# Performance work log

Measured on AMD Instinct MI355X. Metric: run time of the kernel, lower is better.

## Reference

```python
import jax, jax.numpy as jnp
from jax import lax
import numpy as np

B, T, I, H = 256, 1024, 128, 256


def setup_inputs() -> dict:
    key = jax.random.key(0)
    k1, k2, k3 = jax.random.split(key, 3)
    # Xavier-ish scaling so sigmoid/tanh gates are not saturated
    s_ih = float(np.sqrt(2.0 / (I + 3 * H)))
    s_hh = float(np.sqrt(2.0 / (H + 3 * H)))
    return {
        "x": jax.random.normal(k1, (B, T, I), dtype=jnp.float32),
        "h0": jnp.zeros((B, H), dtype=jnp.float32),
        "weight_ih": jax.random.normal(k2, (3 * H, I), dtype=jnp.float32) * s_ih,
        "weight_hh": jax.random.normal(k3, (3 * H, H), dtype=jnp.float32) * s_hh,
        "bias_ih": jnp.zeros((3 * H,), dtype=jnp.float32),
        "bias_hh": jnp.zeros((3 * H,), dtype=jnp.float32),
    }


def reference(x, h0, weight_ih, weight_hh, bias_ih, bias_hh):
    # Precompute batched input-to-hidden GEMM for all timesteps: [B, T, 3H]
    gates_x = jnp.einsum("bti,gi->btg", x, weight_ih) + bias_ih
    gates_x = jnp.swapaxes(gates_x, 0, 1)  # [T, B, 3H] for scan

    def step(h, gx):
        # NOTE: faithful to source — reset gate multiplies the FULL new-gate
        # preactivation (which already includes the hidden contribution),
        # unlike a standard GRU.
        gates = gx + h @ weight_hh.T + bias_hh  # [B, 3H]
        r, z, n = jnp.split(gates, 3, axis=-1)
        r = jax.nn.sigmoid(r)
        z = jax.nn.sigmoid(z)
        n = jnp.tanh(r * n)
        h_new = (1.0 - z) * h + z * n
        return h_new, h_new

    h_last, outs = lax.scan(step, h0, gates_x)  # outs: [T, B, H]
    output = jnp.swapaxes(outs, 0, 1)  # [B, T, H] (batch_first=True)
    return output, h_last
```

## Files before the change

kernel.cpp:

```cpp
#include <hip/hip_runtime.h>


#define B_SZ 256
#define T_SZ 1024
#define H_SZ 256
#define G3   768
#define NGRP 32
#define SPIN_MAX (1 << 27)

template<int CTRL>
__device__ __forceinline__ float dppx(float s) {
    return __int_as_float(
        __builtin_amdgcn_update_dpp(0, __float_as_int(s), CTRL, 0xF, 0xF, true));
}
template<int MASK>
__device__ __forceinline__ float swzx(float s) {
    return __int_as_float(__builtin_amdgcn_ds_swizzle(__float_as_int(s), MASK));
}

static __device__ __forceinline__ int kpad(int k) { return k + 4 * (k >> 4); }

static __device__ __forceinline__ size_t xsl(int g, int par, int n, int u) {
    return (((size_t)g * 2 + par) * 8 + n) * 256 + u;
}

__global__ void prep_kernel(const float* __restrict__ h0,
                            unsigned long long* __restrict__ xch) {
    int tid = blockIdx.x * blockDim.x + threadIdx.x;
    if (tid < B_SZ * H_SZ) {
        int b = tid >> 8, u = tid & 255;
        int g = b >> 3, n = b & 7;
        unsigned long long val = (unsigned long long)__float_as_uint(h0[tid]);
        xch[xsl(g, 0, n, u)] = val;
        xch[xsl(g, 1, n, u)] = val;
    }
}

__global__ __launch_bounds__(256) void gemm_x_kernel(
    const float* __restrict__ x, const float* __restrict__ wih,
    float* __restrict__ gx, int c, int tcShift)
{
    __shared__ __align__(16) float xs[64][132];
    __shared__ __align__(16) float ws[128][68];
    const int TC = 1 << tcShift;
    const int t  = threadIdx.x;
    const int bx = blockIdx.x, by = blockIdx.y;

#pragma unroll
    for (int i = 0; i < 8; ++i) {
        int f4 = t + i * 256;
        int r  = f4 >> 5, c4 = (f4 & 31) * 4;
        int rho = bx * 64 + r;
        int b = rho >> tcShift, u = rho & (TC - 1);
        float4 v = *(const float4*)(x + ((size_t)b * T_SZ + (size_t)c * TC + u) * 128 + c4);
        *(float4*)&xs[r][c4] = v;
    }

    const int gl = t & 31;
    const int rl = t >> 5;
    float acc[8][4];
#pragma unroll
    for (int i = 0; i < 8; ++i)
#pragma unroll
        for (int jj = 0; jj < 4; ++jj) acc[i][jj] = 0.f;

    for (int kb = 0; kb < 2; ++kb) {
        __syncthreads();
#pragma unroll
        for (int i = 0; i < 8; ++i) {
            int f4 = t + i * 256;
            int row = f4 >> 4, c4 = (f4 & 15) * 4;
            float4 v = *(const float4*)(wih + (size_t)(by * 128 + row) * 128 + kb * 64 + c4);
            *(float4*)&ws[row][c4] = v;
        }
        __syncthreads();

#pragma unroll 4
        for (int k4 = 0; k4 < 16; ++k4) {
            float4 wv0 = *(const float4*)&ws[gl     ][k4 * 4];
            float4 wv1 = *(const float4*)&ws[gl + 32][k4 * 4];
            float4 wv2 = *(const float4*)&ws[gl + 64][k4 * 4];
            float4 wv3 = *(const float4*)&ws[gl + 96][k4 * 4];
#pragma unroll
            for (int rr = 0; rr < 8; ++rr) {
                float4 xv = *(const float4*)&xs[rl + rr * 8][kb * 64 + k4 * 4];
                acc[rr][0] = fmaf(xv.w, wv0.w, fmaf(xv.z, wv0.z, fmaf(xv.y, wv0.y, fmaf(xv.x, wv0.x, acc[rr][0]))));
                acc[rr][1] = fmaf(xv.w, wv1.w, fmaf(xv.z, wv1.z, fmaf(xv.y, wv1.y, fmaf(xv.x, wv1.x, acc[rr][1]))));
                acc[rr][2] = fmaf(xv.w, wv2.w, fmaf(xv.z, wv2.z, fmaf(xv.y, wv2.y, fmaf(xv.x, wv2.x, acc[rr][2]))));
                acc[rr][3] = fmaf(xv.w, wv3.w, fmaf(xv.z, wv3.z, fmaf(xv.y, wv3.y, fmaf(xv.x, wv3.x, acc[rr][3]))));
            }
        }
    }

#pragma unroll
    for (int rr = 0; rr < 8; ++rr) {
        size_t base = (size_t)(bx * 64 + rl + rr * 8) * G3 + by * 128 + gl;
#pragma unroll
        for (int gi = 0; gi < 4; ++gi)
            gx[base + 32 * gi] = acc[rr][gi];
    }
}

__device__ __forceinline__ float d8(float a, const float4& Wl, const float4& Wh,
                                    const float4& H0, const float4& H1) {
    a = fmaf(Wl.x, H0.x, a); a = fmaf(Wl.y, H0.y, a);
    a = fmaf(Wl.z, H0.z, a); a = fmaf(Wl.w, H0.w, a);
    a = fmaf(Wh.x, H1.x, a); a = fmaf(Wh.y, H1.y, a);
    a = fmaf(Wh.z, H1.z, a); a = fmaf(Wh.w, H1.w, a);
    return a;
}

#define PIN4(v) asm volatile("" : "+v"(v.x), "+v"(v.y), "+v"(v.z), "+v"(v.w));

__global__ __launch_bounds__(512)
__attribute__((amdgpu_waves_per_eu(2, 2)))
void gru_kernel(
    const float* __restrict__ gx, const float* __restrict__ whh,
    const float* __restrict__ bih, const float* __restrict__ bhh,
    unsigned long long* __restrict__ xch, float* __restrict__ out,
    int gbase, int tc, int isLast)
{
    __shared__ __align__(16) float hl[8][320];
    __shared__ __align__(16) float hst[8][32];

    const int t   = threadIdx.x;
    const int bid = blockIdx.x;
    const int g   = bid & 31;
    const int w   = bid >> 5;
    const int u0  = w * 32;
    const int j2  = t >> 5;
    const int p   = t & 31;
    const int ua  = u0 + 2 * j2;
    const int ub  = ua + 1;
    const int k0  = 8 * p;

    float4 a0l = *(const float4*)(whh + (size_t)(ua)       * H_SZ + k0);
    float4 a0h = *(const float4*)(whh + (size_t)(ua)       * H_SZ + k0 + 4);
    float4 a1l = *(const float4*)(whh + (size_t)(256 + ua) * H_SZ + k0);
    float4 a1h = *(const float4*)(whh + (size_t)(256 + ua) * H_SZ + k0 + 4);
    float4 a2l = *(const float4*)(whh + (size_t)(512 + ua) * H_SZ + k0);
    float4 a2h = *(const float4*)(whh + (size_t)(512 + ua) * H_SZ + k0 + 4);
    float4 c0l = *(const float4*)(whh + (size_t)(ub)       * H_SZ + k0);
    float4 c0h = *(const float4*)(whh + (size_t)(ub)       * H_SZ + k0 + 4);
    float4 c1l = *(const float4*)(whh + (size_t)(256 + ub) * H_SZ + k0);
    float4 c1h = *(const float4*)(whh + (size_t)(256 + ub) * H_SZ + k0 + 4);
    float4 c2l = *(const float4*)(whh + (size_t)(512 + ub) * H_SZ + k0);
    float4 c2h = *(const float4*)(whh + (size_t)(512 + ub) * H_SZ + k0 + 4);
    PIN4(a0l) PIN4(a0h) PIN4(a1l) PIN4(a1h) PIN4(a2l) PIN4(a2h)
    PIN4(c0l) PIN4(c0h) PIN4(c1l) PIN4(c1h) PIN4(c2l) PIN4(c2h)

    const float bsrA = bih[ua]       + bhh[ua];
    const float bszA = bih[256 + ua] + bhh[256 + ua];
    const float bsnA = bih[512 + ua] + bhh[512 + ua];
    const float bsrB = bih[ub]       + bhh[ub];
    const float bszB = bih[256 + ub] + bhh[256 + ub];
    const float bsnB = bih[512 + ub] + bhh[512 + ub];

    const float* gxp = (p < 8) ? gx + ((size_t)(8 * g + p) * tc) * G3 + ua : nullptr;

    const int n_t = t >> 6;
    const int c_t = 4 * (t & 63);
    const int kct = kpad(c_t);
    const int kp8 = kpad(k0);
    const int kua = kpad(ua);
    const int n_o = t >> 3, f_o = t & 7;

    const bool kb0 = (p & 1) != 0, kb1 = (p & 2) != 0, kb2 = (p & 4) != 0;

    float gxrA = 0.f, gxzA = 0.f, gxnA = 0.f, gxrB = 0.f, gxzB = 0.f, gxnB = 0.f;
    if (p < 8) {
        gxrA = gxp[0];   gxzA = gxp[256]; gxnA = gxp[512];
        gxrB = gxp[1];   gxzB = gxp[257]; gxnB = gxp[513];
    }

#pragma unroll 1
    for (int u = 0; u < tc; ++u) {
        const int tg  = gbase + u;
        const int par = tg & 1;

        if (u > 0 && t < 64) {
            float4 o;
            o.x = hst[n_o][4 * f_o];     o.y = hst[n_o][4 * f_o + 1];
            o.z = hst[n_o][4 * f_o + 2]; o.w = hst[n_o][4 * f_o + 3];
            *(float4*)(out + ((size_t)(8 * g + n_o) * T_SZ + (tg - 1)) * H_SZ + u0 + 4 * f_o) = o;
        }

        {
            unsigned long long* sb = xch + xsl(g, par, n_t, c_t);
            const unsigned want = (unsigned)tg;
            unsigned long long v0, v1, v2, v3;
            int sp = 0;
            for (;;) {
                v0 = __hip_atomic_load(sb + 0, __ATOMIC_RELAXED, __HIP_MEMORY_SCOPE_AGENT);
                v1 = __hip_atomic_load(sb + 1, __ATOMIC_RELAXED, __HIP_MEMORY_SCOPE_AGENT);
                v2 = __hip_atomic_load(sb + 2, __ATOMIC_RELAXED, __HIP_MEMORY_SCOPE_AGENT);
                v3 = __hip_atomic_load(sb + 3, __ATOMIC_RELAXED, __HIP_MEMORY_SCOPE_AGENT);
                bool ok = ((unsigned)(v0 >> 32) == want) & ((unsigned)(v1 >> 32) == want) &
                          ((unsigned)(v2 >> 32) == want) & ((unsigned)(v3 >> 32) == want);
                if (ok || ++sp >= SPIN_MAX) break;
                __builtin_amdgcn_s_sleep(2);
            }
            float4 hv;
            hv.x = __uint_as_float((unsigned)v0);
            hv.y = __uint_as_float((unsigned)v1);
            hv.z = __uint_as_float((unsigned)v2);
            hv.w = __uint_as_float((unsigned)v3);
            *(float4*)&hl[n_t][kct] = hv;
        }
        __syncthreads();

        float pgrA = 0.f, pgzA = 0.f, pgnA = 0.f, pgrB = 0.f, pgzB = 0.f, pgnB = 0.f;
        if (p < 8 && u + 1 < tc) {
            size_t go = (size_t)(u + 1) * G3;
            pgrA = gxp[go];     pgzA = gxp[go + 256]; pgnA = gxp[go + 512];
            pgrB = gxp[go + 1]; pgzB = gxp[go + 257]; pgnB = gxp[go + 513];
        }

        float aA0[8], aA1[8], aA2[8], aB0[8], aB1[8], aB2[8];
#pragma unroll
        for (int n = 0; n < 8; ++n) {
            float4 h0v = *(const float4*)&hl[n][kp8];
            float4 h1v = *(const float4*)&hl[n][kp8 + 4];
            aA0[n] = d8(0.f, a0l, a0h, h0v, h1v);
            aA1[n] = d8(0.f, a1l, a1h, h0v, h1v);
            aA2[n] = d8(0.f, a2l, a2h, h0v, h1v);
            aB0[n] = d8(0.f, c0l, c0h, h0v, h1v);
            aB1[n] = d8(0.f, c1l, c1h, h0v, h1v);
            aB2[n] = d8(0.f, c2l, c2h, h0v, h1v);
        }

        float r1A0[4], r1A1[4], r1A2[4], r1B0[4], r1B1[4], r1B2[4];
#pragma unroll
        for (int i = 0; i < 4; ++i) {
            float K, S;
            K = kb0 ? aA0[2*i+1] : aA0[2*i]; S = kb0 ? aA0[2*i] : aA0[2*i+1];
            r1A0[i] = K + dppx<0xB1>(S);
            K = kb0 ? aA1[2*i+1] : aA1[2*i]; S = kb0 ? aA1[2*i] : aA1[2*i+1];
            r1A1[i] = K + dppx<0xB1>(S);
            K = kb0 ? aA2[2*i+1] : aA2[2*i]; S = kb0 ? aA2[2*i] : aA2[2*i+1];
            r1A2[i] = K + dppx<0xB1>(S);
            K = kb0 ? aB0[2*i+1] : aB0[2*i]; S = kb0 ? aB0[2*i] : aB0[2*i+1];
            r1B0[i] = K + dppx<0xB1>(S);
            K = kb0 ? aB1[2*i+1] : aB1[2*i]; S = kb0 ? aB1[2*i] : aB1[2*i+1];
            r1B1[i] = K + dppx<0xB1>(S);
            K = kb0 ? aB2[2*i+1] : aB2[2*i]; S = kb0 ? aB2[2*i] : aB2[2*i+1];
            r1B2[i] = K + dppx<0xB1>(S);
        }
        float r2A0[2], r2A1[2], r2A2[2], r2B0[2], r2B1[2], r2B2[2];
#pragma unroll
        for (int i = 0; i < 2; ++i) {
            float K, S;
            K = kb1 ? r1A0[2*i+1] : r1A0[2*i]; S = kb1 ? r1A0[2*i] : r1A0[2*i+1];
            r2A0[i] = K + dppx<0x4E>(S);
            K = kb1 ? r1A1[2*i+1] : r1A1[2*i]; S = kb1 ? r1A1[2*i] : r1A1[2*i+1];
            r2A1[i] = K + dppx<0x4E>(S);
            K = kb1 ? r1A2[2*i+1] : r1A2[2*i]; S = kb1 ? r1A2[2*i] : r1A2[2*i+1];
            r2A2[i] = K + dppx<0x4E>(S);
            K = kb1 ? r1B0[2*i+1] : r1B0[2*i]; S = kb1 ? r1B0[2*i] : r1B0[2*i+1];
            r2B0[i] = K + dppx<0x4E>(S);
            K = kb1 ? r1B1[2*i+1] : r1B1[2*i]; S = kb1 ? r1B1[2*i] : r1B1[2*i+1];
            r2B1[i] = K + dppx<0x4E>(S);
            K = kb1 ? r1B2[2*i+1] : r1B2[2*i]; S = kb1 ? r1B2[2*i] : r1B2[2*i+1];
            r2B2[i] = K + dppx<0x4E>(S);
        }
        float sA0, sA1, sA2, sB0, sB1, sB2;
        {
            float K, S;
            K = kb2 ? r2A0[1] : r2A0[0]; S = kb2 ? r2A0[0] : r2A0[1];
            sA0 = K + swzx<0x101F>(S);
            K = kb2 ? r2A1[1] : r2A1[0]; S = kb2 ? r2A1[0] : r2A1[1];
            sA1 = K + swzx<0x101F>(S);
            K = kb2 ? r2A2[1] : r2A2[0]; S = kb2 ? r2A2[0] : r2A2[1];
            sA2 = K + swzx<0x101F>(S);
            K = kb2 ? r2B0[1] : r2B0[0]; S = kb2 ? r2B0[0] : r2B0[1];
            sB0 = K + swzx<0x101F>(S);
            K = kb2 ? r2B1[1] : r2B1[0]; S = kb2 ? r2B1[0] : r2B1[1];
            sB1 = K + swzx<0x101F>(S);
            K = kb2 ? r2B2[1] : r2B2[0]; S = kb2 ? r2B2[0] : r2B2[1];
            sB2 = K + swzx<0x101F>(S);
        }
        sA0 += dppx<0x128>(sA0); sA1 += dppx<0x128>(sA1); sA2 += dppx<0x128>(sA2);
        sB0 += dppx<0x128>(sB0); sB1 += dppx<0x128>(sB1); sB2 += dppx<0x128>(sB2);
        sA0 += swzx<0x401F>(sA0); sA1 += swzx<0x401F>(sA1); sA2 += swzx<0x401F>(sA2);
        sB0 += swzx<0x401F>(sB0); sB1 += swzx<0x401F>(sB1); sB2 += swzx<0x401F>(sB2);

        if (p < 8) {
            float holdA = hl[p][kua];
            float holdB = hl[p][kua + 1];
            float arA = sA0 + gxrA + bsrA;
            float azA = sA1 + gxzA + bszA;
            float anA = sA2 + gxnA + bsnA;
            float arB = sB0 + gxrB + bsrB;
            float azB = sB1 + gxzB + bszB;
            float anB = sB2 + gxnB + bsnB;
            float rA = 1.f / (1.f + expf(-arA));
            float zA = 1.f / (1.f + expf(-azA));
            float nA = tanhf(rA * anA);
            float rB = 1.f / (1.f + expf(-arB));
            float zB = 1.f / (1.f + expf(-azB));
            float nB = tanhf(rB * anB);
            float hnA = (1.f - zA) * holdA + zA * nA;
            float hnB = (1.f - zB) * holdB + zB * nB;

            hst[p][2 * j2]     = hnA;
            hst[p][2 * j2 + 1] = hnB;
            const unsigned long long ver = (unsigned long long)(unsigned)(tg + 1) << 32;
            const int par1 = (tg + 1) & 1;
            __hip_atomic_store(xch + xsl(g, par1, p, ua),
                               ver | (unsigned long long)__float_as_uint(hnA),
                               __ATOMIC_RELAXED, __HIP_MEMORY_SCOPE_AGENT);
            __hip_atomic_store(xch + xsl(g, par1, p, ub),
                               ver | (unsigned long long)__float_as_uint(hnB),
                               __ATOMIC_RELAXED, __HIP_MEMORY_SCOPE_AGENT);
        }
        gxrA = pgrA; gxzA = pgzA; gxnA = pgnA;
        gxrB = pgrB; gxzB = pgzB; gxnB = pgnB;
        __syncthreads();
    }

    if (t < 64) {
        float4 o;
        o.x = hst[n_o][4 * f_o];     o.y = hst[n_o][4 * f_o + 1];
        o.z = hst[n_o][4 * f_o + 2]; o.w = hst[n_o][4 * f_o + 3];
        *(float4*)(out + ((size_t)(8 * g + n_o) * T_SZ + (gbase + tc - 1)) * H_SZ + u0 + 4 * f_o) = o;
        if (isLast)
            *(float4*)(out + (size_t)B_SZ * T_SZ * H_SZ
                           + (size_t)(8 * g + n_o) * H_SZ + u0 + 4 * f_o) = o;
    }
}

extern "C" void kernel_launch(void* const* d_in, const int* in_sizes, int n_in,
                              void* d_out, int out_size, void* d_ws, size_t ws_size,
                              hipStream_t stream) {
    const float* x   = (const float*)d_in[0];
    const float* h0  = (const float*)d_in[1];
    const float* wih = (const float*)d_in[2];
    const float* whh = (const float*)d_in[3];
    const float* bih = (const float*)d_in[4];
    const float* bhh = (const float*)d_in[5];
    float* out = (float*)d_out;

    char* ws = (char*)d_ws;
    const size_t xchB = (size_t)NGRP * 2 * 8 * 256 * 8;
    unsigned long long* xch = (unsigned long long*)ws;
    float* gxb = (float*)(ws + xchB);

    int tcShift = 10;
    while (tcShift > 0 &&
           xchB + (786432ull << tcShift) > ws_size) --tcShift;
    const int TC  = 1 << tcShift;
    const int nCh = T_SZ / TC;

    prep_kernel<<<dim3(256), dim3(256), 0, stream>>>(h0, xch);
    for (int c = 0; c < nCh; ++c) {
        gemm_x_kernel<<<dim3(B_SZ * TC / 64, 6), dim3(256), 0, stream>>>(
            x, wih, gxb, c, tcShift);
        gru_kernel<<<dim3(B_SZ), dim3(512), 0, stream>>>(
            gxb, whh, bih, bhh, xch, out, c * TC, TC, (c == nCh - 1) ? 1 : 0);
    }
}
```

Before: 4.006 ms.

## Use packed FP32 FMA and XOR-rotated hidden rows to simplify cross-lane reduction

The recurrent matvec now keeps weights as float2 pairs and uses v_pk_fma_f32, halving the FMA instruction count. Each lane reads hidden-state rows in an XOR-permuted order (i ^ (p&7)), so the butterfly reduction no longer needs per-lane select swaps before each DPP/swizzle step. The LDS padding layout is also changed to pad every 32 floats, to avoid bank conflicts under the new access pattern. The risk lies in the correctness of the reduction index mapping and in the extra register pressure or pack/unpack moves that packed math may introduce.

```diff
diff --git a/kernel.cpp b/kernel.cpp
--- a/kernel.cpp
+++ b/kernel.cpp
@@ -7,6 +7,9 @@
 #define G3   768
 #define NGRP 32
 #define SPIN_MAX (1 << 27)
+#define HROW 288
+
+typedef __attribute__((ext_vector_type(2))) float f32x2;
 
 template<int CTRL>
 __device__ __forceinline__ float dppx(float s) {
@@ -17,8 +20,13 @@
 __device__ __forceinline__ float swzx(float s) {
     return __int_as_float(__builtin_amdgcn_ds_swizzle(__float_as_int(s), MASK));
 }
-
-static __device__ __forceinline__ int kpad(int k) { return k + 4 * (k >> 4); }
+__device__ __forceinline__ f32x2 pkfma(f32x2 a, f32x2 b, f32x2 c) {
+    f32x2 d;
+    asm("v_pk_fma_f32 %0, %1, %2, %3" : "=v"(d) : "v"(a), "v"(b), "v"(c));
+    return d;
+}
+
+static __device__ __forceinline__ int hpos(int k) { return k + 4 * (k >> 5); }
 
 static __device__ __forceinline__ size_t xsl(int g, int par, int n, int u) {
     return (((size_t)g * 2 + par) * 8 + n) * 256 + u;
@@ -101,16 +109,7 @@
     }
 }
 
-__device__ __forceinline__ float d8(float a, const float4& Wl, const float4& Wh,
-                                    const float4& H0, const float4& H1) {
-    a = fmaf(Wl.x, H0.x, a); a = fmaf(Wl.y, H0.y, a);
-    a = fmaf(Wl.z, H0.z, a); a = fmaf(Wl.w, H0.w, a);
-    a = fmaf(Wh.x, H1.x, a); a = fmaf(Wh.y, H1.y, a);
-    a = fmaf(Wh.z, H1.z, a); a = fmaf(Wh.w, H1.w, a);
-    return a;
-}
-
-#define PIN4(v) asm volatile("" : "+v"(v.x), "+v"(v.y), "+v"(v.z), "+v"(v.w));
+#define PIN2(v) asm volatile("" : "+v"(v));
 
 __global__ __launch_bounds__(512)
 __attribute__((amdgpu_waves_per_eu(2, 2)))
@@ -120,7 +119,7 @@
     unsigned long long* __restrict__ xch, float* __restrict__ out,
     int gbase, int tc, int isLast)
 {
-    __shared__ __align__(16) float hl[8][320];
+    __shared__ __align__(16) float hl[8][HROW];
     __shared__ __align__(16) float hst[8][32];
 
     const int t   = threadIdx.x;
@@ -130,24 +129,28 @@
     const int u0  = w * 32;
     const int j2  = t >> 5;
     const int p   = t & 31;
+    const int pb  = p & 7;
     const int ua  = u0 + 2 * j2;
     const int ub  = ua + 1;
     const int k0  = 8 * p;
 
-    float4 a0l = *(const float4*)(whh + (size_t)(ua)       * H_SZ + k0);
-    float4 a0h = *(const float4*)(whh + (size_t)(ua)       * H_SZ + k0 + 4);
-    float4 a1l = *(const float4*)(whh + (size_t)(256 + ua) * H_SZ + k0);
-    float4 a1h = *(const float4*)(whh + (size_t)(256 + ua) * H_SZ + k0 + 4);
-    float4 a2l = *(const float4*)(whh + (size_t)(512 + ua) * H_SZ + k0);
-    float4 a2h = *(const float4*)(whh + (size_t)(512 + ua) * H_SZ + k0 + 4);
-    float4 c0l = *(const float4*)(whh + (size_t)(ub)       * H_SZ + k0);
-    float4 c0h = *(const float4*)(whh + (size_t)(ub)       * H_SZ + k0 + 4);
-    float4 c1l = *(const float4*)(whh + (size_t)(256 + ub) * H_SZ + k0);
-    float4 c1h = *(const float4*)(whh + (size_t)(256 + ub) * H_SZ + k0 + 4);
-    float4 c2l = *(const float4*)(whh + (size_t)(512 + ub) * H_SZ + k0);
-    float4 c2h = *(const float4*)(whh + (size_t)(512 + ub) * H_SZ + k0 + 4);
-    PIN4(a0l) PIN4(a0h) PIN4(a1l) PIN4(a1h) PIN4(a2l) PIN4(a2h)
-    PIN4(c0l) PIN4(c0h) PIN4(c1l) PIN4(c1h) PIN4(c2l) PIN4(c2h)
+    f32x2 wf[6][4];
+    {
+        const int rows[6] = {ua, 256 + ua, 512 + ua, ub, 256 + ub, 512 + ub};
+#pragma unroll
+        for (int f = 0; f < 6; ++f) {
+            float4 va = *(const float4*)(whh + (size_t)rows[f] * H_SZ + k0);
+            float4 vb = *(const float4*)(whh + (size_t)rows[f] * H_SZ + k0 + 4);
+            wf[f][0] = (f32x2){va.x, va.y};
+            wf[f][1] = (f32x2){va.z, va.w};
+            wf[f][2] = (f32x2){vb.x, vb.y};
+            wf[f][3] = (f32x2){vb.z, vb.w};
+        }
+    }
+#pragma unroll
+    for (int f = 0; f < 6; ++f) {
+        PIN2(wf[f][0]) PIN2(wf[f][1]) PIN2(wf[f][2]) PIN2(wf[f][3])
+    }
 
     const float bsrA = bih[ua]       + bhh[ua];
     const float bszA = bih[256 + ua] + bhh[256 + ua];
@@ -159,13 +162,14 @@
     const float* gxp = (p < 8) ? gx + ((size_t)(8 * g + p) * tc) * G3 + ua : nullptr;
 
     const int n_t = t >> 6;
-    const int c_t = 4 * (t & 63);
-    const int kct = kpad(c_t);
-    const int kp8 = kpad(k0);
-    const int kua = kpad(ua);
+    const int m   = t & 63;
+    const int wofs = 4 * m + 4 * (m >> 3);
+    const int Wd = hpos(k0);
+    const float* hrow[8];
+#pragma unroll
+    for (int i = 0; i < 8; ++i) hrow[i] = &hl[i ^ pb][Wd];
+    const int pua = hpos(ua);
     const int n_o = t >> 3, f_o = t & 7;
-
-    const bool kb0 = (p & 1) != 0, kb1 = (p & 2) != 0, kb2 = (p & 4) != 0;
 
     float gxrA = 0.f, gxzA = 0.f, gxnA = 0.f, gxrB = 0.f, gxzB = 0.f, gxnB = 0.f;
     if (p < 8) {
@@ -186,7 +190,7 @@
         }
 
         {
-            unsigned long long* sb = xch + xsl(g, par, n_t, c_t);
+            unsigned long long* sb = xch + xsl(g, par, n_t, 4 * m);
             const unsigned want = (unsigned)tg;
             unsigned long long v0, v1, v2, v3;
             int sp = 0;
@@ -205,7 +209,7 @@
             hv.y = __uint_as_float((unsigned)v1);
             hv.z = __uint_as_float((unsigned)v2);
             hv.w = __uint_as_float((unsigned)v3);
-            *(float4*)&hl[n_t][kct] = hv;
+            *(float4*)&hl[n_t][wofs] = hv;
         }
         __syncthreads();
 
@@ -216,83 +220,58 @@
             pgrB = gxp[go + 1]; pgzB = gxp[go + 257]; pgnB = gxp[go + 513];
         }
 
-        float aA0[8], aA1[8], aA2[8], aB0[8], aB1[8], aB2[8];
-#pragma unroll
-        for (int n = 0; n < 8; ++n) {
-            float4 h0v = *(const float4*)&hl[n][kp8];
-            float4 h1v = *(const float4*)&hl[n][kp8 + 4];
-            aA0[n] = d8(0.f, a0l, a0h, h0v, h1v);
-            aA1[n] = d8(0.f, a1l, a1h, h0v, h1v);
-            aA2[n] = d8(0.f, a2l, a2h, h0v, h1v);
-            aB0[n] = d8(0.f, c0l, c0h, h0v, h1v);
-            aB1[n] = d8(0.f, c1l, c1h, h0v, h1v);
-            aB2[n] = d8(0.f, c2l, c2h, h0v, h1v);
-        }
-
-        float r1A0[4], r1A1[4], r1A2[4], r1B0[4], r1B1[4], r1B2[4];
-#pragma unroll
-        for (int i = 0; i < 4; ++i) {
-            float K, S;
-            K = kb0 ? aA0[2*i+1] : aA0[2*i]; S = kb0 ? aA0[2*i] : aA0[2*i+1];
-            r1A0[i] = K + dppx<0xB1>(S);
-            K = kb0 ? aA1[2*i+1] : aA1[2*i]; S = kb0 ? aA1[2*i] : aA1[2*i+1];
-            r1A1[i] = K + dppx<0xB1>(S);
-            K = kb0 ? aA2[2*i+1] : aA2[2*i]; S = kb0 ? aA2[2*i] : aA2[2*i+1];
-            r1A2[i] = K + dppx<0xB1>(S);
-            K = kb0 ? aB0[2*i+1] : aB0[2*i]; S = kb0 ? aB0[2*i] : aB0[2*i+1];
-            r1B0[i] = K + dppx<0xB1>(S);
-            K = kb0 ? aB1[2*i+1] : aB1[2*i]; S = kb0 ? aB1[2*i] : aB1[2*i+1];
-            r1B1[i] = K + dppx<0xB1>(S);
-            K = kb0 ? aB2[2*i+1] : aB2[2*i]; S = kb0 ? aB2[2*i] : aB2[2*i+1];
-            r1B2[i] = K + dppx<0xB1>(S);
-        }
-        float r2A0[2], r2A1[2], r2A2[2], r2B0[2], r2B1[2], r2B2[2];
-#pragma unroll
-        for (int i = 0; i < 2; ++i) {
-            float K, S;
-            K = kb1 ? r1A0[2*i+1] : r1A0[2*i]; S = kb1 ? r1A0[2*i] : r1A0[2*i+1];
-            r2A0[i] = K + dppx<0x4E>(S);
-            K = kb1 ? r1A1[2*i+1] : r1A1[2*i]; S = kb1 ? r1A1[2*i] : r1A1[2*i+1];
-            r2A1[i] = K + dppx<0x4E>(S);
-            K = kb1 ? r1A2[2*i+1] : r1A2[2*i]; S = kb1 ? r1A2[2*i] : r1A2[2*i+1];
-            r2A2[i] = K + dppx<0x4E>(S);
-            K = kb1 ? r1B0[2*i+1] : r1B0[2*i]; S = kb1 ? r1B0[2*i] : r1B0[2*i+1];
-            r2B0[i] = K + dppx<0x4E>(S);
-            K = kb1 ? r1B1[2*i+1] : r1B1[2*i]; S = kb1 ? r1B1[2*i] : r1B1[2*i+1];
-            r2B1[i] = K + dppx<0x4E>(S);
-            K = kb1 ? r1B2[2*i+1] : r1B2[2*i]; S = kb1 ? r1B2[2*i] : r1B2[2*i+1];
-            r2B2[i] = K + dppx<0x4E>(S);
-        }
-        float sA0, sA1, sA2, sB0, sB1, sB2;
-        {
-            float K, S;
-            K = kb2 ? r2A0[1] : r2A0[0]; S = kb2 ? r2A0[0] : r2A0[1];
-            sA0 = K + swzx<0x101F>(S);
-            K = kb2 ? r2A1[1] : r2A1[0]; S = kb2 ? r2A1[0] : r2A1[1];
-            sA1 = K + swzx<0x101F>(S);
-            K = kb2 ? r2A2[1] : r2A2[0]; S = kb2 ? r2A2[0] : r2A2[1];
-            sA2 = K + swzx<0x101F>(S);
-            K = kb2 ? r2B0[1] : r2B0[0]; S = kb2 ? r2B0[0] : r2B0[1];
-            sB0 = K + swzx<0x101F>(S);
-            K = kb2 ? r2B1[1] : r2B1[0]; S = kb2 ? r2B1[0] : r2B1[1];
-            sB1 = K + swzx<0x101F>(S);
-            K = kb2 ? r2B2[1] : r2B2[0]; S = kb2 ? r2B2[0] : r2B2[1];
-            sB2 = K + swzx<0x101F>(S);
-        }
-        sA0 += dppx<0x128>(sA0); sA1 += dppx<0x128>(sA1); sA2 += dppx<0x128>(sA2);
-        sB0 += dppx<0x128>(sB0); sB1 += dppx<0x128>(sB1); sB2 += dppx<0x128>(sB2);
-        sA0 += swzx<0x401F>(sA0); sA1 += swzx<0x401F>(sA1); sA2 += swzx<0x401F>(sA2);
-        sB0 += swzx<0x401F>(sB0); sB1 += swzx<0x401F>(sB1); sB2 += swzx<0x401F>(sB2);
+        float s0[8], s1[8], s2[8], s3[8], s4[8], s5[8];
+#pragma unroll
+        for (int i = 0; i < 8; ++i) {
+            const float* hr = hrow[i];
+            float4 hv0 = *(const float4*)(hr);
+            float4 hv1 = *(const float4*)(hr + 4);
+            f32x2 h0 = (f32x2){hv0.x, hv0.y};
+            f32x2 h1 = (f32x2){hv0.z, hv0.w};
+            f32x2 h2 = (f32x2){hv1.x, hv1.y};
+            f32x2 h3 = (f32x2){hv1.z, hv1.w};
+            f32x2 z = (f32x2){0.f, 0.f};
+            f32x2 a0 = pkfma(h0, wf[0][0], pkfma(h1, wf[0][1], pkfma(h2, wf[0][2], pkfma(h3, wf[0][3], z))));
+            f32x2 a1 = pkfma(h0, wf[1][0], pkfma(h1, wf[1][1], pkfma(h2, wf[1][2], pkfma(h3, wf[1][3], z))));
+            f32x2 a2 = pkfma(h0, wf[2][0], pkfma(h1, wf[2][1], pkfma(h2, wf[2][2], pkfma(h3, wf[2][3], z))));
+            f32x2 a3 = pkfma(h0, wf[3][0], pkfma(h1, wf[3][1], pkfma(h2, wf[3][2], pkfma(h3, wf[3][3], z))));
+            f32x2 a4 = pkfma(h0, wf[4][0], pkfma(h1, wf[4][1], pkfma(h2, wf[4][2], pkfma(h3, wf[4][3], z))));
+            f32x2 a5 = pkfma(h0, wf[5][0], pkfma(h1, wf[5][1], pkfma(h2, wf[5][2], pkfma(h3, wf[5][3], z))));
+            s0[i] = a0.x + a0.y; s1[i] = a1.x + a1.y; s2[i] = a2.x + a2.y;
+            s3[i] = a3.x + a3.y; s4[i] = a4.x + a4.y; s5[i] = a5.x + a5.y;
+        }
+
+#pragma unroll
+        for (int i = 0; i < 8; i += 2) {
+            s0[i] += dppx<0xB1>(s0[i ^ 1]); s1[i] += dppx<0xB1>(s1[i ^ 1]);
+            s2[i] += dppx<0xB1>(s2[i ^ 1]); s3[i] += dppx<0xB1>(s3[i ^ 1]);
+            s4[i] += dppx<0xB1>(s4[i ^ 1]); s5[i] += dppx<0xB1>(s5[i ^ 1]);
+        }
+#pragma unroll
+        for (int i = 0; i < 8; i += 4) {
+            s0[i] += dppx<0x4E>(s0[i ^ 2]); s1[i] += dppx<0x4E>(s1[i ^ 2]);
+            s2[i] += dppx<0x4E>(s2[i ^ 2]); s3[i] += dppx<0x4E>(s3[i ^ 2]);
+            s4[i] += dppx<0x4E>(s4[i ^ 2]); s5[i] += dppx<0x4E>(s5[i ^ 2]);
+        }
+        s0[0] += swzx<0x101F>(s0[4]); s1[0] += swzx<0x101F>(s1[4]);
+        s2[0] += swzx<0x101F>(s2[4]); s3[0] += swzx<0x101F>(s3[4]);
+        s4[0] += swzx<0x101F>(s4[4]); s5[0] += swzx<0x101F>(s5[4]);
+        s0[0] += dppx<0x128>(s0[0]); s1[0] += dppx<0x128>(s1[0]);
+        s2[0] += dppx<0x128>(s2[0]); s3[0] += dppx<0x128>(s3[0]);
+        s4[0] += dppx<0x128>(s4[0]); s5[0] += dppx<0x128>(s5[0]);
+        s0[0] += swzx<0x401F>(s0[0]); s1[0] += swzx<0x401F>(s1[0]);
+        s2[0] += swzx<0x401F>(s2[0]); s3[0] += swzx<0x401F>(s3[0]);
+        s4[0] += swzx<0x401F>(s4[0]); s5[0] += swzx<0x401F>(s5[0]);
 
         if (p < 8) {
-            float holdA = hl[p][kua];
-            float holdB = hl[p][kua + 1];
-            float arA = sA0 + gxrA + bsrA;
-            float azA = sA1 + gxzA + bszA;
-            float anA = sA2 + gxnA + bsnA;
-            float arB = sB0 + gxrB + bsrB;
-            float azB = sB1 + gxzB + bszB;
-            float anB = sB2 + gxnB + bsnB;
+            float holdA = hl[p][pua];
+            float holdB = hl[p][pua + 1];
+            float arA = s0[0] + gxrA + bsrA;
+            float azA = s1[0] + gxzA + bszA;
+            float anA = s2[0] + gxnA + bsnA;
+            float arB = s3[0] + gxrB + bsrB;
+            float azB = s4[0] + gxzB + bszB;
+            float anB = s5[0] + gxnB + bsnB;
             float rA = 1.f / (1.f + expf(-arA));
             float zA = 1.f / (1.f + expf(-azA));
             float nA = tanhf(rA * anA);
```

New measurement: 4.060 ms. Within noise of the previous version (+1.4%).
